# Performance work log

Hardware: AMD Instinct MI355X
Metric: run time of the kernel (lower is better)

## Reference

```python
import jax, jax.numpy as jnp
import numpy as np

N = 100000
E = 1600000
EPS = 1e-5


def setup_inputs() -> dict:
    key = jax.random.key(0)
    ks = jax.random.split(key, 6)
    x = jax.random.normal(ks[0], (N, 128), dtype=jnp.float32)
    edge_index = jax.random.randint(ks[1], (2, E), 0, N, dtype=jnp.int64)
    # Glorot-ish scaled weights
    W1 = jax.random.normal(ks[2], (128, 128), dtype=jnp.float32) * (1.0 / np.sqrt(128))
    b1 = jnp.zeros((128,), dtype=jnp.float32)
    gamma = jnp.ones((128,), dtype=jnp.float32)
    beta = jnp.zeros((128,), dtype=jnp.float32)
    W2 = jax.random.normal(ks[3], (64, 128), dtype=jnp.float32) * (1.0 / np.sqrt(128))
    b2 = jnp.zeros((64,), dtype=jnp.float32)
    return {"x": x, "edge_index": edge_index, "W1": W1, "b1": b1,
            "gamma": gamma, "beta": beta, "W2": W2, "b2": b2}


def _gcn_conv(x, W, b, src, dst, norm, n):
    # x: [N, Fin], W: [Fout, Fin] -> h: [N, Fout]
    h = x @ W.T
    msg = h[src] * norm[:, None]               # [E+N, Fout] gather + scale
    out = jax.ops.segment_sum(msg, dst, num_segments=n)  # scatter-add
    return out + b


def reference(x, edge_index, W1, b1, gamma, beta, W2, b2):
    n = x.shape[0]
    loop = jnp.arange(n, dtype=edge_index.dtype)
    src = jnp.concatenate([edge_index[0], loop])   # self-loops appended
    dst = jnp.concatenate([edge_index[1], loop])
    # symmetric normalization D^-1/2 A D^-1/2 (degree at destination)
    deg = jax.ops.segment_sum(jnp.ones_like(dst, dtype=x.dtype), dst, num_segments=n)
    dis = jnp.where(deg > 0, jax.lax.rsqrt(deg), 0.0)
    norm = dis[src] * dis[dst]

    h = _gcn_conv(x, W1, b1, src, dst, norm, n)
    # BatchNorm1d (training mode: biased batch statistics over nodes)
    mean = jnp.mean(h, axis=0)
    var = jnp.mean((h - mean) ** 2, axis=0)
    h = (h - mean) * jax.lax.rsqrt(var + EPS) * gamma + beta
    h = jax.nn.relu(h)
    out = _gcn_conv(h, W2, b2, src, dst, norm, n)
    return out
```

## Files before the change

### kernel.cpp

```cpp
#include <hip/hip_runtime.h>


#define SHIFT 8
#define BSZ   256
#define CHUNK 4096
#define EPT   (CHUNK/256)
#define NBMAX 1024

typedef short bf16x8 __attribute__((ext_vector_type(8)));
typedef float f32x4  __attribute__((ext_vector_type(4)));

__device__ __forceinline__ unsigned short f2bf(float f) {
    unsigned int u = __float_as_uint(f);
    unsigned int r = (u + 0x7FFFu + ((u >> 16) & 1u)) >> 16;
    return (unsigned short)r;
}
__device__ __forceinline__ float bf2f(unsigned short h) {
    return __uint_as_float(((unsigned int)h) << 16);
}
__device__ __forceinline__ void split2(float a, float b, unsigned int& hi, unsigned int& lo) {
    unsigned int ua = __float_as_uint(a), ub = __float_as_uint(b);
    unsigned int ha = ua & 0xFFFF0000u,  hb = ub & 0xFFFF0000u;
    hi = (ha >> 16) | hb;
    float la = a - __uint_as_float(ha);
    float lb = b - __uint_as_float(hb);
    lo = (__float_as_uint(la) >> 16) | (__float_as_uint(lb) & 0xFFFF0000u);
}
__device__ __forceinline__ int detect64(const int* __restrict__ p) {
    int o = 0;
#pragma unroll
    for (int q = 0; q < 16; ++q) o |= p[2 * q + 1];
    return (o == 0) ? 1 : 0;
}

__global__ __launch_bounds__(256) void k_prep(const float* __restrict__ W1,
                                              const float* __restrict__ W2,
                                              uint4* __restrict__ Whi1,
                                              uint4* __restrict__ Wlo1,
                                              uint4* __restrict__ Whi2,
                                              uint4* __restrict__ Wlo2,
                                              int* __restrict__ gcnt,
                                              float* __restrict__ spart) {
    int gid = blockIdx.x * 256 + threadIdx.x;
    if (gid < 1024) gcnt[gid] = 0;
    for (int u = gid; u < 16384; u += 4096) spart[u] = 0.f;
    const float* W; uint4 *H, *L; int slot;
    if (gid < 2048)      { W = W1; H = Whi1; L = Wlo1; slot = gid; }
    else if (gid < 3072) { W = W2; H = Whi2; L = Wlo2; slot = gid - 2048; }
    else return;
    int lane = slot & 63, kt = (slot >> 6) & 3, nt = slot >> 8;
    int o = nt * 16 + (lane & 15);
    int k0 = kt * 32 + (lane >> 4) * 8;
    const float* p = W + (size_t)o * 128 + k0;
    unsigned int h[4], l[4];
#pragma unroll
    for (int pr = 0; pr < 4; ++pr) split2(p[2 * pr], p[2 * pr + 1], h[pr], l[pr]);
    H[slot] = make_uint4(h[0], h[1], h[2], h[3]);
    L[slot] = make_uint4(l[0], l[1], l[2], l[3]);
}

__global__ __launch_bounds__(256) void k_hist(const void* __restrict__ eiv,
                                              int* __restrict__ gcnt,
                                              int E, int N, int NB) {
    __shared__ int h[NBMAX];
    int t = threadIdx.x;
    for (int u = t; u < NB; u += 256) h[u] = 0;
    __syncthreads();
    int base = blockIdx.x * CHUNK;
    int f = detect64((const int*)eiv);
    const long long* e64 = (const long long*)eiv;
    const int*       e32 = (const int*)eiv;
#pragma unroll
    for (int r = 0; r < EPT; ++r) {
        int e = base + r * 256 + t;
        if (e < E) {
            int s, d;
            if (f) { s = (int)e64[e]; d = (int)e64[E + e]; }
            else   { s = e32[e];      d = e32[E + e]; }
            if ((unsigned)s < (unsigned)N && (unsigned)d < (unsigned)N)
                atomicAdd(&h[d >> SHIFT], 1);
        }
    }
    __syncthreads();
    for (int u = t; u < NB; u += 256) {
        int c = h[u];
        if (c) atomicAdd(&gcnt[u], c);
    }
}

__global__ void k_scan(const int* __restrict__ gcnt, int* __restrict__ gbase,
                       int* __restrict__ gcur, int NB) {
    __shared__ int sh[1024];
    int t = threadIdx.x;
    int v = (t < NB) ? gcnt[t] : 0;
    sh[t] = v;
    __syncthreads();
    for (int off = 1; off < 1024; off <<= 1) {
        int x = sh[t];
        int y = (t >= off) ? sh[t - off] : 0;
        __syncthreads();
        sh[t] = x + y;
        __syncthreads();
    }
    if (t < NB) {
        int ex = sh[t] - v;
        gbase[t] = ex;
        gcur[t]  = ex;
    }
    if (t == 0) gbase[NB] = sh[1023];
}

__global__ __launch_bounds__(256) void k_scatter(const void* __restrict__ eiv,
                                                 int* __restrict__ gcur,
                                                 unsigned int* __restrict__ ebuf,
                                                 int E, int N, int NB) {
    __shared__ int lcnt[NBMAX];
    __shared__ int lbase[NBMAX];
    int t = threadIdx.x;
    for (int u = t; u < NB; u += 256) lcnt[u] = 0;
    __syncthreads();
    int base = blockIdx.x * CHUNK;
    int f = detect64((const int*)eiv);
    const long long* e64 = (const long long*)eiv;
    const int*       e32 = (const int*)eiv;
    unsigned int ent[EPT];
    int bk[EPT];
    int off[EPT];
#pragma unroll
    for (int r = 0; r < EPT; ++r) {
        int e = base + r * 256 + t;
        bk[r] = -1;
        if (e < E) {
            int s, d;
            if (f) { s = (int)e64[e]; d = (int)e64[E + e]; }
            else   { s = e32[e];      d = e32[E + e]; }
            if ((unsigned)s < (unsigned)N && (unsigned)d < (unsigned)N) {
                int b = d >> SHIFT;
                bk[r]  = b;
                off[r] = atomicAdd(&lcnt[b], 1);
                ent[r] = ((unsigned int)(d & (BSZ - 1)) << 24) | (unsigned int)s;
            }
        }
    }
    __syncthreads();
    for (int u = t; u < NB; u += 256) {
        int c = lcnt[u];
        lbase[u] = c ? atomicAdd(&gcur[u], c) : 0;
    }
    __syncthreads();
#pragma unroll
    for (int r = 0; r < EPT; ++r)
        if (bk[r] >= 0) ebuf[(size_t)lbase[bk[r]] + off[r]] = ent[r];
}

__global__ __launch_bounds__(256) void k_fine(const unsigned int* __restrict__ ebuf,
                                              const int* __restrict__ gbase,
                                              int* __restrict__ cnt,
                                              float* __restrict__ dis,
                                              int* __restrict__ rowptr,
                                              int* __restrict__ elist, int N) {
    __shared__ int lc[BSZ];
    __shared__ int ls[BSZ];
    int t = threadIdx.x;
    int b = blockIdx.x;
    int start = gbase[b], end = gbase[b + 1];
    int m = end - start;
    lc[t] = 0;
    __syncthreads();
    for (int j = t; j < m; j += 256)
        atomicAdd(&lc[ebuf[start + j] >> 24], 1);
    __syncthreads();
    int v = lc[t];
    ls[t] = v;
    __syncthreads();
    for (int off = 1; off < BSZ; off <<= 1) {
        int x = ls[t];
        int y = (t >= off) ? ls[t - off] : 0;
        __syncthreads();
        ls[t] = x + y;
        __syncthreads();
    }
    int ex = ls[t] - v;
    int i = (b << SHIFT) + t;
    if (i < N) {
        cnt[i]    = v;
        dis[i]    = rsqrtf((float)v + 1.0f);
        rowptr[i] = start + ex;
    }
    lc[t] = ex;
    __syncthreads();
    for (int j = t; j < m; j += 256) {
        unsigned int e = ebuf[start + j];
        int p = atomicAdd(&lc[e >> 24], 1);
        elist[start + p] = (int)(e & 0xFFFFFFu);
    }
}

__global__ __launch_bounds__(256) void k_gemm1(const float* __restrict__ x,
                                               const uint4* __restrict__ Whi,
                                               const uint4* __restrict__ Wlo,
                                               const float* __restrict__ dis,
                                               unsigned short* __restrict__ h1b, int N) {
    __shared__ uint4 Ahi[1024];
    __shared__ uint4 Alo[1024];
    int t = threadIdx.x;
    int n0 = blockIdx.x * 64;
    for (int s = t; s < 1024; s += 256) {
        int lane = s & 63, kt = (s >> 6) & 3, c = s >> 8;
        int row = n0 + c * 16 + (lane & 15);
        int rr = min(row, N - 1);
        int k0 = kt * 32 + (lane >> 4) * 8;
        const float4* p = (const float4*)(x + (size_t)rr * 128 + k0);
        float4 u0 = p[0], u1 = p[1];
        unsigned int h0, h1, h2, h3, l0, l1, l2, l3;
        split2(u0.x, u0.y, h0, l0);
        split2(u0.z, u0.w, h1, l1);
        split2(u1.x, u1.y, h2, l2);
        split2(u1.z, u1.w, h3, l3);
        Ahi[s] = make_uint4(h0, h1, h2, h3);
        Alo[s] = make_uint4(l0, l1, l2, l3);
    }
    __syncthreads();
    int w = t >> 6, lane = t & 63;
    bf16x8 ah[4], al[4];
#pragma unroll
    for (int kt = 0; kt < 4; ++kt) {
        ah[kt] = ((const bf16x8*)Ahi)[(w * 4 + kt) * 64 + lane];
        al[kt] = ((const bf16x8*)Alo)[(w * 4 + kt) * 64 + lane];
    }
    f32x4 acc[8];
#pragma unroll
    for (int nt = 0; nt < 8; ++nt) {
        acc[nt] = (f32x4)(0.f);
#pragma unroll
        for (int kt = 0; kt < 4; ++kt) {
            bf16x8 bh = ((const bf16x8*)Whi)[(nt * 4 + kt) * 64 + lane];
            bf16x8 bl = ((const bf16x8*)Wlo)[(nt * 4 + kt) * 64 + lane];
            acc[nt] = __builtin_amdgcn_mfma_f32_16x16x32_bf16(ah[kt], bh, acc[nt], 0, 0, 0);
            acc[nt] = __builtin_amdgcn_mfma_f32_16x16x32_bf16(ah[kt], bl, acc[nt], 0, 0, 0);
            acc[nt] = __builtin_amdgcn_mfma_f32_16x16x32_bf16(al[kt], bh, acc[nt], 0, 0, 0);
        }
    }
    int r0 = n0 + w * 16 + (lane >> 4) * 4;
    float dv[4];
#pragma unroll
    for (int r = 0; r < 4; ++r) {
        int row = r0 + r;
        dv[r] = (row < N) ? dis[row] : 0.f;
    }
#pragma unroll
    for (int nt = 0; nt < 8; ++nt) {
        int col = nt * 16 + (lane & 15);
#pragma unroll
        for (int r = 0; r < 4; ++r) {
            int row = r0 + r;
            if (row < N) h1b[(size_t)row * 128 + col] = f2bf(dv[r] * acc[nt][r]);
        }
    }
}

__global__ __launch_bounds__(256) void k_agg1(const unsigned int* __restrict__ h1b,
                                              const float* __restrict__ dis,
                                              const int* __restrict__ rowptr,
                                              const int* __restrict__ cnt,
                                              const int* __restrict__ elist,
                                              float* __restrict__ agg1,
                                              float* __restrict__ spart, int N) {
    int t = threadIdx.x;
    int lane = t & 63;
    int i0 = blockIdx.x * 16 + (t >> 6) * 4;
    float sx = 0.f, sy = 0.f, qx = 0.f, qy = 0.f;
#pragma unroll
    for (int k = 0; k < 4; ++k) {
        int i = i0 + k;
        bool act = (i < N);
        float accx = 0.f, accy = 0.f;
        int base = 0, c = 0;
        if (act) { base = rowptr[i]; c = cnt[i]; }
        int j = 0;
        for (; j + 16 <= c; j += 16) {
            int ss[16];
#pragma unroll
            for (int r = 0; r < 16; ++r) ss[r] = elist[base + j + r];
            unsigned int vv[16];
#pragma unroll
            for (int r = 0; r < 16; ++r) vv[r] = h1b[(size_t)ss[r] * 64 + lane];
#pragma unroll
            for (int r = 0; r < 16; ++r) {
                accx += bf2f((unsigned short)(vv[r] & 0xFFFF));
                accy += bf2f((unsigned short)(vv[r] >> 16));
            }
        }
        if (j + 8 <= c) {
            int ss[8];
#pragma unroll
            for (int r = 0; r < 8; ++r) ss[r] = elist[base + j + r];
            unsigned int vv[8];
#pragma unroll
            for (int r = 0; r < 8; ++r) vv[r] = h1b[(size_t)ss[r] * 64 + lane];
#pragma unroll
            for (int r = 0; r < 8; ++r) {
                accx += bf2f((unsigned short)(vv[r] & 0xFFFF));
                accy += bf2f((unsigned short)(vv[r] >> 16));
            }
            j += 8;
        }
        for (; j < c; ++j) {
            int s = elist[base + j];
            unsigned int v = h1b[(size_t)s * 64 + lane];
            accx += bf2f((unsigned short)(v & 0xFFFF));
            accy += bf2f((unsigned short)(v >> 16));
        }
        if (act) {
            float di = dis[i];
            unsigned int sv = h1b[(size_t)i * 64 + lane];
            float rx = di * (accx + bf2f((unsigned short)(sv & 0xFFFF)));
            float ry = di * (accy + bf2f((unsigned short)(sv >> 16)));
            ((float2*)agg1)[(size_t)i * 64 + lane] = make_float2(rx, ry);
            sx += rx; sy += ry; qx += rx * rx; qy += ry * ry;
        }
    }
    __shared__ float4 red[256];
    red[t] = make_float4(sx, sy, qx, qy);
    __syncthreads();
    if (t < 64) {
        float4 a = red[t], b = red[t + 64], cc = red[t + 128], d = red[t + 192];
        float ssx = a.x + b.x + cc.x + d.x;
        float ssy = a.y + b.y + cc.y + d.y;
        float sqx = a.z + b.z + cc.z + d.z;
        float sqy = a.w + b.w + cc.w + d.w;
        float* sp = spart + ((size_t)(blockIdx.x & 63) << 8);
        atomicAdd(&sp[2 * t],           ssx);
        atomicAdd(&sp[2 * t + 1],       ssy);
        atomicAdd(&sp[128 + 2 * t],     sqx);
        atomicAdd(&sp[128 + 2 * t + 1], sqy);
    }
}

__global__ __launch_bounds__(256) void k_gemm2(const float* __restrict__ agg1,
                                               const uint4* __restrict__ Whi,
                                               const uint4* __restrict__ Wlo,
                                               const float* __restrict__ spart,
                                               const float* __restrict__ gamma,
                                               const float* __restrict__ beta,
                                               const float* __restrict__ dis,
                                               unsigned short* __restrict__ h2b, int N) {
    __shared__ uint4 Ahi[1024];
    __shared__ uint4 Alo[1024];
    __shared__ float sred[256];
    __shared__ float bnsc[128], bnsh[128];
    int t = threadIdx.x;
    int n0 = blockIdx.x * 64;
    {
        float s = 0.f;
        for (int sl = 0; sl < 64; ++sl) s += spart[sl * 256 + t];
        sred[t] = s;
        __syncthreads();
        if (t < 128) {
            float invN = 1.0f / (float)N;
            float mean = sred[t] * invN;
            float var = sred[128 + t] * invN - mean * mean;
            var = fmaxf(var, 0.f);
            float inv = rsqrtf(var + 1e-5f);
            float sc = gamma[t] * inv;
            bnsc[t] = sc;
            bnsh[t] = beta[t] - mean * sc;
        }
        __syncthreads();
    }
    for (int s = t; s < 1024; s += 256) {
        int lane = s & 63, kt = (s >> 6) & 3, c = s >> 8;
        int row = n0 + c * 16 + (lane & 15);
        int rr = min(row, N - 1);
        int k0 = kt * 32 + (lane >> 4) * 8;
        const float4* p = (const float4*)(agg1 + (size_t)rr * 128 + k0);
        float4 a0 = p[0], a1 = p[1];
        float v0 = fmaxf(a0.x * bnsc[k0 + 0] + bnsh[k0 + 0], 0.f);
        float v1 = fmaxf(a0.y * bnsc[k0 + 1] + bnsh[k0 + 1], 0.f);
        float v2 = fmaxf(a0.z * bnsc[k0 + 2] + bnsh[k0 + 2], 0.f);
        float v3 = fmaxf(a0.w * bnsc[k0 + 3] + bnsh[k0 + 3], 0.f);
        float v4 = fmaxf(a1.x * bnsc[k0 + 4] + bnsh[k0 + 4], 0.f);
        float v5 = fmaxf(a1.y * bnsc[k0 + 5] + bnsh[k0 + 5], 0.f);
        float v6 = fmaxf(a1.z * bnsc[k0 + 6] + bnsh[k0 + 6], 0.f);
        float v7 = fmaxf(a1.w * bnsc[k0 + 7] + bnsh[k0 + 7], 0.f);
        unsigned int h0, h1, h2, h3, l0, l1, l2, l3;
        split2(v0, v1, h0, l0);
        split2(v2, v3, h1, l1);
        split2(v4, v5, h2, l2);
        split2(v6, v7, h3, l3);
        Ahi[s] = make_uint4(h0, h1, h2, h3);
        Alo[s] = make_uint4(l0, l1, l2, l3);
    }
    __syncthreads();
    int w = t >> 6, lane = t & 63;
    bf16x8 ah[4], al[4];
#pragma unroll
    for (int kt = 0; kt < 4; ++kt) {
        ah[kt] = ((const bf16x8*)Ahi)[(w * 4 + kt) * 64 + lane];
        al[kt] = ((const bf16x8*)Alo)[(w * 4 + kt) * 64 + lane];
    }
    f32x4 acc[4];
#pragma unroll
    for (int nt = 0; nt < 4; ++nt) {
        acc[nt] = (f32x4)(0.f);
#pragma unroll
        for (int kt = 0; kt < 4; ++kt) {
            bf16x8 bh = ((const bf16x8*)Whi)[(nt * 4 + kt) * 64 + lane];
            bf16x8 bl = ((const bf16x8*)Wlo)[(nt * 4 + kt) * 64 + lane];
            acc[nt] = __builtin_amdgcn_mfma_f32_16x16x32_bf16(ah[kt], bh, acc[nt], 0, 0, 0);
            acc[nt] = __builtin_amdgcn_mfma_f32_16x16x32_bf16(ah[kt], bl, acc[nt], 0, 0, 0);
            acc[nt] = __builtin_amdgcn_mfma_f32_16x16x32_bf16(al[kt], bh, acc[nt], 0, 0, 0);
        }
    }
    int r0 = n0 + w * 16 + (lane >> 4) * 4;
    float dv[4];
#pragma unroll
    for (int r = 0; r < 4; ++r) {
        int row = r0 + r;
        dv[r] = (row < N) ? dis[row] : 0.f;
    }
#pragma unroll
    for (int nt = 0; nt < 4; ++nt) {
        int col = nt * 16 + (lane & 15);
#pragma unroll
        for (int r = 0; r < 4; ++r) {
            int row = r0 + r;
            if (row < N) h2b[(size_t)row * 64 + col] = f2bf(dv[r] * acc[nt][r]);
        }
    }
}

__global__ __launch_bounds__(256) void k_agg2(const unsigned short* __restrict__ h2b,
                                              const float* __restrict__ dis,
                                              const int* __restrict__ rowptr,
                                              const int* __restrict__ cnt,
                                              const int* __restrict__ elist,
                                              const float* __restrict__ b2,
                                              float* __restrict__ out, int N) {
    int lane = threadIdx.x & 63;
    int i = blockIdx.x * 4 + (threadIdx.x >> 6);
    if (i >= N) return;
    float acc = 0.f;
    int base = rowptr[i], c = cnt[i];
    int j = 0;
    for (; j + 16 <= c; j += 16) {
        int ss[16];
#pragma unroll
        for (int r = 0; r < 16; ++r) ss[r] = elist[base + j + r];
        unsigned short vv[16];
#pragma unroll
        for (int r = 0; r < 16; ++r) vv[r] = h2b[(size_t)ss[r] * 64 + lane];
#pragma unroll
        for (int r = 0; r < 16; ++r) acc += bf2f(vv[r]);
    }
    if (j + 8 <= c) {
        int ss[8];
#pragma unroll
        for (int r = 0; r < 8; ++r) ss[r] = elist[base + j + r];
        unsigned short vv[8];
#pragma unroll
        for (int r = 0; r < 8; ++r) vv[r] = h2b[(size_t)ss[r] * 64 + lane];
#pragma unroll
        for (int r = 0; r < 8; ++r) acc += bf2f(vv[r]);
        j += 8;
    }
    for (; j < c; ++j) {
        int s = elist[base + j];
        acc += bf2f(h2b[(size_t)s * 64 + lane]);
    }
    float di = dis[i];
    float self = bf2f(h2b[(size_t)i * 64 + lane]);
    out[(size_t)i * 64 + lane] = di * (acc + self) + b2[lane];
}

extern "C" void kernel_launch(void* const* d_in, const int* in_sizes, int n_in,
                              void* d_out, int out_size, void* d_ws, size_t ws_size,
                              hipStream_t stream) {
    const float* x     = (const float*)d_in[0];
    const void*  ei    = d_in[1];
    const float* W1    = (const float*)d_in[2];
    const float* gamma = (const float*)d_in[4];
    const float* beta  = (const float*)d_in[5];
    const float* W2    = (const float*)d_in[6];
    const float* b2    = (const float*)d_in[7];
    float* out = (float*)d_out;

    int N = in_sizes[0] / 128;
    int E = in_sizes[1] / 2;
    int NB = (N + BSZ - 1) >> SHIFT;

    size_t Na = ((size_t)N + 3) & ~(size_t)3;
    size_t Ea = ((size_t)E + 3) & ~(size_t)3;
    int*   cnt    = (int*)d_ws;
    int*   rowptr = cnt + Na;
    int*   gcnt   = rowptr + Na;
    int*   gbase  = gcnt + 1024;
    int*   gcur   = gbase + 1028;
    float* stats  = (float*)(gcur + 1024);
    float* spart  = stats + 512;
    float* dis    = spart + 65536;
    int*   elist  = (int*)(dis + Na);
    unsigned int* h1b = (unsigned int*)(elist + Ea);
    float* agg1   = (float*)(h1b + Na * 64);
    unsigned int* ebuf = (unsigned int*)agg1;
    uint4* Whi1   = (uint4*)(agg1 + Na * 128);
    uint4* Wlo1   = Whi1 + 2048;
    uint4* Whi2   = Wlo1 + 2048;
    uint4* Wlo2   = Whi2 + 1024;
    unsigned int* h2b = h1b;

    int gC    = (E + CHUNK - 1) / CHUNK;
    int gG1   = (N + 63) / 64;
    int gAgg1 = (N + 15) / 16;
    int gAgg2 = (N + 3) / 4;

    k_prep<<<16, 256, 0, stream>>>(W1, W2, Whi1, Wlo1, Whi2, Wlo2, gcnt, spart);
    k_hist<<<gC, 256, 0, stream>>>(ei, gcnt, E, N, NB);
    k_scan<<<1, 1024, 0, stream>>>(gcnt, gbase, gcur, NB);
    k_scatter<<<gC, 256, 0, stream>>>(ei, gcur, ebuf, E, N, NB);
    k_fine<<<NB, 256, 0, stream>>>(ebuf, gbase, cnt, dis, rowptr, elist, N);
    k_gemm1<<<gG1, 256, 0, stream>>>(x, Whi1, Wlo1, dis, (unsigned short*)h1b, N);
    k_agg1<<<gAgg1, 256, 0, stream>>>(h1b, dis, rowptr, cnt, elist, agg1, spart, N);
    k_gemm2<<<gG1, 256, 0, stream>>>(agg1, Whi2, Wlo2, spart, gamma, beta, dis, (unsigned short*)h2b, N);
    k_agg2<<<gAgg2, 256, 0, stream>>>((const unsigned short*)h2b, dis, rowptr, cnt, elist, b2, out, N);
}
```

Baseline: 381.7 us.

## Widen gather loads in aggregation kernels and fuse scan into histogram

Aggregation kernels now split each wave across several edges, with each lane loading 8 bytes of bf16 features; partial sums are combined via cross-lane shuffles. This aims to cut the number of load instructions and raise memory parallelism for the irregular gathers. The separate single-block scan kernel is removed: the last histogram block, detected via an atomic counter, performs the prefix scan. This saves a launch at the cost of a threadfence and a counter that aliases the unused stats area.

```diff
diff --git a/kernel.cpp b/kernel.cpp
--- a/kernel.cpp
+++ b/kernel.cpp
@@ -40,9 +40,11 @@
                                               uint4* __restrict__ Whi2,
                                               uint4* __restrict__ Wlo2,
                                               int* __restrict__ gcnt,
-                                              float* __restrict__ spart) {
+                                              float* __restrict__ spart,
+                                              int* __restrict__ done) {
     int gid = blockIdx.x * 256 + threadIdx.x;
     if (gid < 1024) gcnt[gid] = 0;
+    if (gid == 0) done[0] = 0;
     for (int u = gid; u < 16384; u += 4096) spart[u] = 0.f;
     const float* W; uint4 *H, *L; int slot;
     if (gid < 2048)      { W = W1; H = Whi1; L = Wlo1; slot = gid; }
@@ -61,8 +63,13 @@
 
 __global__ __launch_bounds__(256) void k_hist(const void* __restrict__ eiv,
                                               int* __restrict__ gcnt,
+                                              int* __restrict__ gbase,
+                                              int* __restrict__ gcur,
+                                              int* __restrict__ done,
                                               int E, int N, int NB) {
     __shared__ int h[NBMAX];
+    __shared__ int ssum[256];
+    __shared__ int lastflag;
     int t = threadIdx.x;
     for (int u = t; u < NB; u += 256) h[u] = 0;
     __syncthreads();
@@ -86,28 +93,29 @@
         int c = h[u];
         if (c) atomicAdd(&gcnt[u], c);
     }
-}
-
-__global__ void k_scan(const int* __restrict__ gcnt, int* __restrict__ gbase,
-                       int* __restrict__ gcur, int NB) {
-    __shared__ int sh[1024];
-    int t = threadIdx.x;
-    int v = (t < NB) ? gcnt[t] : 0;
-    sh[t] = v;
-    __syncthreads();
-    for (int off = 1; off < 1024; off <<= 1) {
-        int x = sh[t];
-        int y = (t >= off) ? sh[t - off] : 0;
+    __threadfence();
+    if (t == 0) lastflag = (atomicAdd(done, 1) == (int)gridDim.x - 1) ? 1 : 0;
+    __syncthreads();
+    if (!lastflag) return;
+    __threadfence();
+    int v0 = gcnt[4 * t], v1 = gcnt[4 * t + 1], v2 = gcnt[4 * t + 2], v3 = gcnt[4 * t + 3];
+    int tsum = v0 + v1 + v2 + v3;
+    ssum[t] = tsum;
+    __syncthreads();
+    for (int o = 1; o < 256; o <<= 1) {
+        int x = ssum[t];
+        int y = (t >= o) ? ssum[t - o] : 0;
         __syncthreads();
-        sh[t] = x + y;
+        ssum[t] = x + y;
         __syncthreads();
     }
-    if (t < NB) {
-        int ex = sh[t] - v;
-        gbase[t] = ex;
-        gcur[t]  = ex;
-    }
-    if (t == 0) gbase[NB] = sh[1023];
+    int ex = ssum[t] - tsum;
+    int e0 = ex, e1 = ex + v0, e2 = e1 + v1, e3 = e2 + v2;
+    gbase[4 * t] = e0;     gcur[4 * t] = e0;
+    gbase[4 * t + 1] = e1; gcur[4 * t + 1] = e1;
+    gbase[4 * t + 2] = e2; gcur[4 * t + 2] = e2;
+    gbase[4 * t + 3] = e3; gcur[4 * t + 3] = e3;
+    if (t == 255) gbase[NB] = ssum[255];
 }
 
 __global__ __launch_bounds__(256) void k_scatter(const void* __restrict__ eiv,
@@ -268,13 +276,16 @@
                                               float* __restrict__ spart, int N) {
     int t = threadIdx.x;
     int lane = t & 63;
+    int q = lane & 31;
+    int half = lane >> 5;
     int i0 = blockIdx.x * 16 + (t >> 6) * 4;
-    float sx = 0.f, sy = 0.f, qx = 0.f, qy = 0.f;
+    float s0 = 0.f, s1 = 0.f, s2 = 0.f, s3 = 0.f;
+    float q0 = 0.f, q1 = 0.f, q2 = 0.f, q3 = 0.f;
 #pragma unroll
     for (int k = 0; k < 4; ++k) {
         int i = i0 + k;
         bool act = (i < N);
-        float accx = 0.f, accy = 0.f;
+        float f0 = 0.f, f1 = 0.f, f2 = 0.f, f3 = 0.f;
         int base = 0, c = 0;
         if (act) { base = rowptr[i]; c = cnt[i]; }
         int j = 0;
@@ -282,58 +293,92 @@
             int ss[16];
 #pragma unroll
             for (int r = 0; r < 16; ++r) ss[r] = elist[base + j + r];
-            unsigned int vv[16];
-#pragma unroll
-            for (int r = 0; r < 16; ++r) vv[r] = h1b[(size_t)ss[r] * 64 + lane];
-#pragma unroll
-            for (int r = 0; r < 16; ++r) {
-                accx += bf2f((unsigned short)(vv[r] & 0xFFFF));
-                accy += bf2f((unsigned short)(vv[r] >> 16));
+            uint2 vv[8];
+#pragma unroll
+            for (int r = 0; r < 8; ++r)
+                vv[r] = *(const uint2*)(h1b + (size_t)ss[2 * r + half] * 64 + 2 * q);
+#pragma unroll
+            for (int r = 0; r < 8; ++r) {
+                f0 += bf2f((unsigned short)(vv[r].x & 0xFFFF));
+                f1 += bf2f((unsigned short)(vv[r].x >> 16));
+                f2 += bf2f((unsigned short)(vv[r].y & 0xFFFF));
+                f3 += bf2f((unsigned short)(vv[r].y >> 16));
             }
         }
         if (j + 8 <= c) {
             int ss[8];
 #pragma unroll
             for (int r = 0; r < 8; ++r) ss[r] = elist[base + j + r];
-            unsigned int vv[8];
-#pragma unroll
-            for (int r = 0; r < 8; ++r) vv[r] = h1b[(size_t)ss[r] * 64 + lane];
-#pragma unroll
-            for (int r = 0; r < 8; ++r) {
-                accx += bf2f((unsigned short)(vv[r] & 0xFFFF));
-                accy += bf2f((unsigned short)(vv[r] >> 16));
+            uint2 vv[4];
+#pragma unroll
+            for (int r = 0; r < 4; ++r)
+                vv[r] = *(const uint2*)(h1b + (size_t)ss[2 * r + half] * 64 + 2 * q);
+#pragma unroll
+            for (int r = 0; r < 4; ++r) {
+                f0 += bf2f((unsigned short)(vv[r].x & 0xFFFF));
+                f1 += bf2f((unsigned short)(vv[r].x >> 16));
+                f2 += bf2f((unsigned short)(vv[r].y & 0xFFFF));
+                f3 += bf2f((unsigned short)(vv[r].y >> 16));
             }
             j += 8;
         }
-        for (; j < c; ++j) {
+        if (j + 2 <= c) {
+            int n2 = (c - j) >> 1;
+            for (int p = 0; p < n2; ++p) {
+                int s = elist[base + j + 2 * p + half];
+                uint2 v = *(const uint2*)(h1b + (size_t)s * 64 + 2 * q);
+                f0 += bf2f((unsigned short)(v.x & 0xFFFF));
+                f1 += bf2f((unsigned short)(v.x >> 16));
+                f2 += bf2f((unsigned short)(v.y & 0xFFFF));
+                f3 += bf2f((unsigned short)(v.y >> 16));
+            }
+            j += 2 * n2;
+        }
+        if (j < c && half == 0) {
             int s = elist[base + j];
-            unsigned int v = h1b[(size_t)s * 64 + lane];
-            accx += bf2f((unsigned short)(v & 0xFFFF));
-            accy += bf2f((unsigned short)(v >> 16));
-        }
+            uint2 v = *(const uint2*)(h1b + (size_t)s * 64 + 2 * q);
+            f0 += bf2f((unsigned short)(v.x & 0xFFFF));
+            f1 += bf2f((unsigned short)(v.x >> 16));
+            f2 += bf2f((unsigned short)(v.y & 0xFFFF));
+            f3 += bf2f((unsigned short)(v.y >> 16));
+        }
+        f0 += __shfl_xor(f0, 32, 64);
+        f1 += __shfl_xor(f1, 32, 64);
+        f2 += __shfl_xor(f2, 32, 64);
+        f3 += __shfl_xor(f3, 32, 64);
         if (act) {
             float di = dis[i];
-            unsigned int sv = h1b[(size_t)i * 64 + lane];
-            float rx = di * (accx + bf2f((unsigned short)(sv & 0xFFFF)));
-            float ry = di * (accy + bf2f((unsigned short)(sv >> 16)));
-            ((float2*)agg1)[(size_t)i * 64 + lane] = make_float2(rx, ry);
-            sx += rx; sy += ry; qx += rx * rx; qy += ry * ry;
-        }
-    }
-    __shared__ float4 red[256];
-    red[t] = make_float4(sx, sy, qx, qy);
-    __syncthreads();
-    if (t < 64) {
-        float4 a = red[t], b = red[t + 64], cc = red[t + 128], d = red[t + 192];
-        float ssx = a.x + b.x + cc.x + d.x;
-        float ssy = a.y + b.y + cc.y + d.y;
-        float sqx = a.z + b.z + cc.z + d.z;
-        float sqy = a.w + b.w + cc.w + d.w;
+            uint2 sv = *(const uint2*)(h1b + (size_t)i * 64 + 2 * q);
+            float r0 = di * (f0 + bf2f((unsigned short)(sv.x & 0xFFFF)));
+            float r1 = di * (f1 + bf2f((unsigned short)(sv.x >> 16)));
+            float r2 = di * (f2 + bf2f((unsigned short)(sv.y & 0xFFFF)));
+            float r3 = di * (f3 + bf2f((unsigned short)(sv.y >> 16)));
+            if (half == 0) {
+                *(float4*)(agg1 + (size_t)i * 128 + 4 * q) = make_float4(r0, r1, r2, r3);
+                s0 += r0; s1 += r1; s2 += r2; s3 += r3;
+                q0 += r0 * r0; q1 += r1 * r1; q2 += r2 * r2; q3 += r3 * r3;
+            }
+        }
+    }
+    __shared__ float4 reds[128], redq[128];
+    int w = t >> 6;
+    if (half == 0) {
+        reds[w * 32 + q] = make_float4(s0, s1, s2, s3);
+        redq[w * 32 + q] = make_float4(q0, q1, q2, q3);
+    }
+    __syncthreads();
+    if (t < 32) {
+        float4 a = reds[t], b = reds[t + 32], c = reds[t + 64], d = reds[t + 96];
+        float4 e = redq[t], f = redq[t + 32], g = redq[t + 64], h = redq[t + 96];
         float* sp = spart + ((size_t)(blockIdx.x & 63) << 8);
-        atomicAdd(&sp[2 * t],           ssx);
-        atomicAdd(&sp[2 * t + 1],       ssy);
-        atomicAdd(&sp[128 + 2 * t],     sqx);
-        atomicAdd(&sp[128 + 2 * t + 1], sqy);
+        atomicAdd(&sp[4 * t + 0],       a.x + b.x + c.x + d.x);
+        atomicAdd(&sp[4 * t + 1],       a.y + b.y + c.y + d.y);
+        atomicAdd(&sp[4 * t + 2],       a.z + b.z + c.z + d.z);
+        atomicAdd(&sp[4 * t + 3],       a.w + b.w + c.w + d.w);
+        atomicAdd(&sp[128 + 4 * t + 0], e.x + f.x + g.x + h.x);
+        atomicAdd(&sp[128 + 4 * t + 1], e.y + f.y + g.y + h.y);
+        atomicAdd(&sp[128 + 4 * t + 2], e.z + f.z + g.z + h.z);
+        atomicAdd(&sp[128 + 4 * t + 3], e.w + f.w + g.w + h.w);
     }
 }
 
@@ -430,7 +475,7 @@
     }
 }
 
-__global__ __launch_bounds__(256) void k_agg2(const unsigned short* __restrict__ h2b,
+__global__ __launch_bounds__(256) void k_agg2(const unsigned int* __restrict__ h2b,
                                               const float* __restrict__ dis,
                                               const int* __restrict__ rowptr,
                                               const int* __restrict__ cnt,
@@ -438,39 +483,65 @@
                                               const float* __restrict__ b2,
                                               float* __restrict__ out, int N) {
     int lane = threadIdx.x & 63;
+    int q = lane & 15;
+    int quad = lane >> 4;
     int i = blockIdx.x * 4 + (threadIdx.x >> 6);
     if (i >= N) return;
-    float acc = 0.f;
+    float f0 = 0.f, f1 = 0.f, f2 = 0.f, f3 = 0.f;
     int base = rowptr[i], c = cnt[i];
     int j = 0;
     for (; j + 16 <= c; j += 16) {
         int ss[16];
 #pragma unroll
         for (int r = 0; r < 16; ++r) ss[r] = elist[base + j + r];
-        unsigned short vv[16];
-#pragma unroll
-        for (int r = 0; r < 16; ++r) vv[r] = h2b[(size_t)ss[r] * 64 + lane];
-#pragma unroll
-        for (int r = 0; r < 16; ++r) acc += bf2f(vv[r]);
-    }
-    if (j + 8 <= c) {
-        int ss[8];
-#pragma unroll
-        for (int r = 0; r < 8; ++r) ss[r] = elist[base + j + r];
-        unsigned short vv[8];
-#pragma unroll
-        for (int r = 0; r < 8; ++r) vv[r] = h2b[(size_t)ss[r] * 64 + lane];
-#pragma unroll
-        for (int r = 0; r < 8; ++r) acc += bf2f(vv[r]);
-        j += 8;
+        uint2 vv[4];
+#pragma unroll
+        for (int r = 0; r < 4; ++r)
+            vv[r] = *(const uint2*)(h2b + (size_t)ss[4 * r + quad] * 32 + 2 * q);
+#pragma unroll
+        for (int r = 0; r < 4; ++r) {
+            f0 += bf2f((unsigned short)(vv[r].x & 0xFFFF));
+            f1 += bf2f((unsigned short)(vv[r].x >> 16));
+            f2 += bf2f((unsigned short)(vv[r].y & 0xFFFF));
+            f3 += bf2f((unsigned short)(vv[r].y >> 16));
+        }
+    }
+    if (j + 4 <= c) {
+        int n4 = (c - j) >> 2;
+        for (int p = 0; p < n4; ++p) {
+            int s = elist[base + j + 4 * p + quad];
+            uint2 v = *(const uint2*)(h2b + (size_t)s * 32 + 2 * q);
+            f0 += bf2f((unsigned short)(v.x & 0xFFFF));
+            f1 += bf2f((unsigned short)(v.x >> 16));
+            f2 += bf2f((unsigned short)(v.y & 0xFFFF));
+            f3 += bf2f((unsigned short)(v.y >> 16));
+        }
+        j += 4 * n4;
     }
     for (; j < c; ++j) {
-        int s = elist[base + j];
-        acc += bf2f(h2b[(size_t)s * 64 + lane]);
-    }
+        if (quad == 0) {
+            int s = elist[base + j];
+            uint2 v = *(const uint2*)(h2b + (size_t)s * 32 + 2 * q);
+            f0 += bf2f((unsigned short)(v.x & 0xFFFF));
+            f1 += bf2f((unsigned short)(v.x >> 16));
+            f2 += bf2f((unsigned short)(v.y & 0xFFFF));
+            f3 += bf2f((unsigned short)(v.y >> 16));
+        }
+    }
+    f0 += __shfl_xor(f0, 16, 64); f0 += __shfl_xor(f0, 32, 64);
+    f1 += __shfl_xor(f1, 16, 64); f1 += __shfl_xor(f1, 32, 64);
+    f2 += __shfl_xor(f2, 16, 64); f2 += __shfl_xor(f2, 32, 64);
+    f3 += __shfl_xor(f3, 16, 64); f3 += __shfl_xor(f3, 32, 64);
     float di = dis[i];
-    float self = bf2f(h2b[(size_t)i * 64 + lane]);
-    out[(size_t)i * 64 + lane] = di * (acc + self) + b2[lane];
+    uint2 sv = *(const uint2*)(h2b + (size_t)i * 32 + 2 * q);
+    if (quad == 0) {
+        float4 bb = ((const float4*)b2)[q];
+        float o0 = di * (f0 + bf2f((unsigned short)(sv.x & 0xFFFF))) + bb.x;
+        float o1 = di * (f1 + bf2f((unsigned short)(sv.x >> 16)))    + bb.y;
+        float o2 = di * (f2 + bf2f((unsigned short)(sv.y & 0xFFFF))) + bb.z;
+        float o3 = di * (f3 + bf2f((unsigned short)(sv.y >> 16)))    + bb.w;
+        *(float4*)(out + (size_t)i * 64 + 4 * q) = make_float4(o0, o1, o2, o3);
+    }
 }
 
 extern "C" void kernel_launch(void* const* d_in, const int* in_sizes, int n_in,
@@ -496,6 +567,7 @@
     int*   gcnt   = rowptr + Na;
     int*   gbase  = gcnt + 1024;
     int*   gcur   = gbase + 1028;
+    int*   done   = gcur + 1024;
     float* stats  = (float*)(gcur + 1024);
     float* spart  = stats + 512;
     float* dis    = spart + 65536;
@@ -514,13 +586,12 @@
     int gAgg1 = (N + 15) / 16;
     int gAgg2 = (N + 3) / 4;
 
-    k_prep<<<16, 256, 0, stream>>>(W1, W2, Whi1, Wlo1, Whi2, Wlo2, gcnt, spart);
-    k_hist<<<gC, 256, 0, stream>>>(ei, gcnt, E, N, NB);
-    k_scan<<<1, 1024, 0, stream>>>(gcnt, gbase, gcur, NB);
+    k_prep<<<16, 256, 0, stream>>>(W1, W2, Whi1, Wlo1, Whi2, Wlo2, gcnt, spart, done);
+    k_hist<<<gC, 256, 0, stream>>>(ei, gcnt, gbase, gcur, done, E, N, NB);
     k_scatter<<<gC, 256, 0, stream>>>(ei, gcur, ebuf, E, N, NB);
     k_fine<<<NB, 256, 0, stream>>>(ebuf, gbase, cnt, dis, rowptr, elist, N);
     k_gemm1<<<gG1, 256, 0, stream>>>(x, Whi1, Wlo1, dis, (unsigned short*)h1b, N);
     k_agg1<<<gAgg1, 256, 0, stream>>>(h1b, dis, rowptr, cnt, elist, agg1, spart, N);
     k_gemm2<<<gG1, 256, 0, stream>>>(agg1, Whi2, Wlo2, spart, gamma, beta, dis, (unsigned short*)h2b, N);
-    k_agg2<<<gAgg2, 256, 0, stream>>>((const unsigned short*)h2b, dis, rowptr, cnt, elist, b2, out, N);
-}
+    k_agg2<<<gAgg2, 256, 0, stream>>>((const unsigned int*)h2b, dis, rowptr, cnt, elist, b2, out, N);
+}
```

After: 398.7 us. +4.5%, slower.
